# Kernel optimization log

Hardware: AMD Instinct MI355X
Metric: run time of the kernel (lower is better)

Reference implementation:

```python
import jax, jax.numpy as jnp
import numpy as np

B, Q, K, H = 8, 2048, 2048, 512


def setup_inputs() -> dict:
    key = jax.random.key(0)
    ks = jax.random.split(key, 12)
    s = 1.0 / np.sqrt(H)
    return {
        "query": jax.random.normal(ks[0], (B, Q, H), jnp.float32),
        "key_": jax.random.normal(ks[1], (B, K, H), jnp.float32),
        "value": jax.random.normal(ks[2], (B, K, H), jnp.float32),
        "mask": jax.random.randint(ks[3], (B, K), 0, 2).astype(bool),
        "Wq": jax.random.normal(ks[4], (H, H), jnp.float32) * s,
        "bq": jnp.zeros((H,), jnp.float32),
        "Wk": jax.random.normal(ks[5], (H, H), jnp.float32) * s,
        "bk": jnp.zeros((H,), jnp.float32),
        "Wv": jax.random.normal(ks[6], (H, H), jnp.float32) * s,
        "bv": jnp.zeros((H,), jnp.float32),
        "Wo": jax.random.normal(ks[7], (H, H), jnp.float32) * s,
        "bo": jnp.zeros((H,), jnp.float32),
    }


def reference(query, key_, value, mask, Wq, bq, Wk, bk, Wv, bv, Wo, bo):
    scale = jnp.sqrt(jnp.float32(H))
    Qp = query @ Wq + bq          # (B,Q,H)
    Kp = key_ @ Wk + bk           # (B,K,H)
    Vp = value @ Wv + bv          # (B,K,H)
    energy = jnp.einsum("bqh,bkh->bqk", Qp, Kp) / scale
    # mask is (B, key_len); torch code broadcasts it over all query rows
    energy = jnp.where(mask[:, None, :], -jnp.inf, energy)
    idx = jnp.argmax(energy, axis=-1)                 # (B,Q)
    score = jax.nn.one_hot(idx, K, dtype=energy.dtype)  # hardmax one-hot (B,Q,K)
    # score @ V is exactly a per-row gather of the argmax-selected V row
    res = jnp.take_along_axis(Vp, idx[:, :, None], axis=1)  # (B,Q,H)
    res = res @ Wo + bo
    return (res, score)
```

## Files before the change

kernel.cpp:

```cpp
#include <hip/hip_runtime.h>

typedef _Float16 f16;
typedef f16 f16x8 __attribute__((ext_vector_type(8)));
typedef f16 f16x4 __attribute__((ext_vector_type(4)));
typedef short s16x8 __attribute__((ext_vector_type(8)));
typedef short s16x4 __attribute__((ext_vector_type(4)));
typedef float f32x4 __attribute__((ext_vector_type(4)));

#define MFMA16(a,b,c)  __builtin_amdgcn_mfma_f32_16x16x32_f16(a,b,c,0,0,0)
#define MFMAB16(a,b,c) __builtin_amdgcn_mfma_f32_16x16x32_bf16(a,b,c,0,0,0)

static constexpr int Bn = 8, Qn = 2048, Kn = 2048, Hn = 512;
static constexpr int Mn = Bn * Qn;

typedef __attribute__((address_space(1))) const unsigned int as1_uint;
typedef __attribute__((address_space(3))) unsigned int as3_uint;

__device__ __forceinline__ void gl_lds16(const void* g, void* l) {
    __builtin_amdgcn_global_load_lds((as1_uint*)g, (as3_uint*)l, 16, 0, 0);
}

__device__ __forceinline__ short bf16r(float x) {
    unsigned u = __builtin_bit_cast(unsigned, x);
    u += 0x7fffu + ((u >> 16) & 1u);
    return (short)(u >> 16);
}

__device__ __forceinline__ int swz(int row) { return (row >> 1) & 3; }

__global__ __launch_bounds__(256) void compact_mask(
    const int* __restrict__ mask, int* __restrict__ cidx, int* __restrict__ cnt)
{
    __shared__ int sums[256];
    int b = blockIdx.x, t = threadIdx.x;
    int base = b * Kn + t * 8;
    int mv[8]; int s = 0;
    #pragma unroll
    for (int i = 0; i < 8; ++i) { mv[i] = (mask[base + i] == 0); s += mv[i]; }
    sums[t] = s;
    __syncthreads();
    for (int off = 1; off < 256; off <<= 1) {
        int v = (t >= off) ? sums[t - off] : 0;
        __syncthreads();
        sums[t] += v;
        __syncthreads();
    }
    int pos = (t > 0 ? sums[t - 1] : 0);
    #pragma unroll
    for (int i = 0; i < 8; ++i)
        if (mv[i]) cidx[b * Kn + pos++] = t * 8 + i;
    if (t == 255) {
        int total = sums[255];
        if (total == 0) { cidx[b * Kn] = 0; total = 1; }
        cnt[b] = total;
    }
}

__global__ __launch_bounds__(256) void prep_split(
    const float* __restrict__ Wk, const float* __restrict__ Wo,
    f16* __restrict__ Wk_h, f16* __restrict__ Wk_l, short* __restrict__ Wot)
{
    int e = blockIdx.x * 256 + threadIdx.x;
    float v = Wk[e] * 512.0f;
    f16 h = (f16)v;
    Wk_h[e] = h; Wk_l[e] = (f16)((v - (float)h) * 2048.0f);
    int r = e >> 9, c = e & 511;
    Wot[c * 512 + r] = bf16r(Wo[e]);
}

__global__ __launch_bounds__(512) void prep_vec(
    const float* __restrict__ Wk, const float* __restrict__ Wo,
    const float* __restrict__ bq, const float* __restrict__ bv,
    const float* __restrict__ bo,
    float* __restrict__ wvec, float* __restrict__ cvec)
{
    int t = threadIdx.x;
    float s = 0.f;
    for (int n = 0; n < 512; n += 4) {
        f32x4 a = *(const f32x4*)(Wk + (size_t)t * 512 + n);
        f32x4 q = *(const f32x4*)(bq + n);
        s += a[0]*q[0] + a[1]*q[1] + a[2]*q[2] + a[3]*q[3];
    }
    wvec[t] = s * (1.0f / 512.0f);
    float s2 = 0.f;
    for (int h = 0; h < 512; ++h) s2 += bv[h] * Wo[h * 512 + t];
    cvec[t] = s2 + bo[t];
}

template<int PREP>
__global__ __launch_bounds__(256) void gemm_split(
    const float* __restrict__ Af,
    const f16* __restrict__ Bh_g, const f16* __restrict__ Bl_g,
    f16* __restrict__ Oh, f16* __restrict__ Ol)
{
    __shared__ __align__(16) f16 Ah[2][2048], Al[2][2048], Bh[2][4096], Bl[2][4096];
    const int tid = threadIdx.x, lane = tid & 63, wid = tid >> 6;
    const int l15 = lane & 15, lg = lane >> 4;
    const int m0 = blockIdx.x * 64, n0 = blockIdx.y * 128;
    const int srow = lane >> 2, sg = lane & 3;
    const int ar0 = tid >> 3, ac0 = (tid & 7) * 4;

    auto stageB = [&](int buf, int ks) {
        const int k0 = ks << 5;
        #pragma unroll
        for (int h = 0; h < 2; ++h) {
            int s = wid + h * 4;
            int row = s * 16 + srow;
            int goff = k0 + ((sg ^ swz(row)) << 3);
            gl_lds16(Bh_g + (size_t)(n0 + row) * Hn + goff, &Bh[buf][s * 512]);
            gl_lds16(Bl_g + (size_t)(n0 + row) * Hn + goff, &Bl[buf][s * 512]);
        }
    };
    auto writeA = [&](int buf, const f32x4* av) {
        #pragma unroll
        for (int rr = 0; rr < 2; ++rr) {
            int row = ar0 + rr * 32;
            f16x4 oh, ol;
            #pragma unroll
            for (int j = 0; j < 4; ++j) {
                f16 hh = (f16)av[rr][j];
                oh[j] = hh;
                ol[j] = (f16)((av[rr][j] - (float)hh) * 2048.0f);
            }
            int off = row * 32 + (((ac0 >> 3) ^ swz(row)) << 3) + (ac0 & 7);
            *(f16x4*)&Ah[buf][off] = oh;
            *(f16x4*)&Al[buf][off] = ol;
        }
    };

    const float* aSrc[2];
    #pragma unroll
    for (int rr = 0; rr < 2; ++rr)
        aSrc[rr] = Af + (size_t)(m0 + ar0 + rr * 32) * Hn;

    f32x4 a0[4][2] = {}, a1[4][2] = {};
    {
        f32x4 av[2];
        #pragma unroll
        for (int rr = 0; rr < 2; ++rr) av[rr] = *(const f32x4*)(aSrc[rr] + ac0);
        stageB(0, 0);
        writeA(0, av);
    }
    __syncthreads();
    #pragma unroll 1
    for (int ks = 0; ks < 16; ++ks) {
        const int cur = ks & 1, nxt = cur ^ 1;
        f32x4 av[2];
        if (ks < 15) {
            const int k1 = (ks + 1) << 5;
            #pragma unroll
            for (int rr = 0; rr < 2; ++rr) av[rr] = *(const f32x4*)(aSrc[rr] + k1 + ac0);
            stageB(nxt, ks + 1);
        }
        f16x8 fbh[2], fbl[2];
        #pragma unroll
        for (int fj = 0; fj < 2; ++fj) {
            int row = wid * 32 + fj * 16 + l15;
            int off = row * 32 + ((lg ^ swz(row)) << 3);
            fbh[fj] = *(f16x8*)&Bh[cur][off];
            fbl[fj] = *(f16x8*)&Bl[cur][off];
        }
        #pragma unroll
        for (int fi = 0; fi < 4; ++fi) {
            int row = fi * 16 + l15;
            int off = row * 32 + ((lg ^ swz(row)) << 3);
            f16x8 fah = *(f16x8*)&Ah[cur][off];
            f16x8 fal = *(f16x8*)&Al[cur][off];
            #pragma unroll
            for (int fj = 0; fj < 2; ++fj) {
                a0[fi][fj] = MFMA16(fah, fbh[fj], a0[fi][fj]);
                a1[fi][fj] = MFMA16(fah, fbl[fj], a1[fi][fj]);
                a1[fi][fj] = MFMA16(fal, fbh[fj], a1[fi][fj]);
            }
        }
        if (ks < 15) writeA(nxt, av);
        __syncthreads();
    }
    #pragma unroll
    for (int fi = 0; fi < 4; ++fi)
    #pragma unroll
    for (int fj = 0; fj < 2; ++fj)
    #pragma unroll
    for (int j = 0; j < 4; ++j) {
        int m = m0 + fi * 16 + lg * 4 + j;
        int n = n0 + wid * 32 + fj * 16 + l15;
        float v = a0[fi][fj][j] + a1[fi][fj][j] * (1.0f / 2048.0f);
        if (PREP == 0) v *= (1.0f / 512.0f);
        f16 h = (f16)v;
        f16 lo = (f16)((v - (float)h) * 2048.0f);
        size_t o = PREP ? ((size_t)n * Hn + m) : ((size_t)m * Hn + n);
        Oh[o] = h; Ol[o] = lo;
    }
}

template<int MODE>
__global__ __launch_bounds__(256) void gemm_bfk(
    const float* __restrict__ Af, const short* __restrict__ Bt,
    const float* __restrict__ cvec, const int* __restrict__ idxArr,
    void* __restrict__ Out)
{
    __shared__ __align__(16) short As[2][2048], Bs[2][4096];
    const int tid = threadIdx.x, lane = tid & 63, wid = tid >> 6;
    const int l15 = lane & 15, lg = lane >> 4;
    const int m0 = blockIdx.x * 64, n0 = blockIdx.y * 128;
    const int srow = lane >> 2, sg = lane & 3;
    const int ar0 = tid >> 3, ac0 = (tid & 7) * 4;

    const float* aSrc[2];
    #pragma unroll
    for (int rr = 0; rr < 2; ++rr) {
        int row = ar0 + rr * 32;
        size_t grow;
        if (MODE == 1) {
            int b = m0 >> 11;
            grow = (size_t)(b * Kn + idxArr[m0 + row]);
        } else {
            grow = (size_t)(m0 + row);
        }
        aSrc[rr] = Af + grow * Hn;
    }

    auto stageB = [&](int buf, int ks) {
        const int k0 = ks << 5;
        #pragma unroll
        for (int h = 0; h < 2; ++h) {
            int s = wid + h * 4;
            int row = s * 16 + srow;
            int goff = k0 + ((sg ^ swz(row)) << 3);
            gl_lds16(Bt + (size_t)(n0 + row) * Hn + goff, &Bs[buf][s * 512]);
        }
    };
    auto writeA = [&](int buf, const f32x4* av) {
        #pragma unroll
        for (int rr = 0; rr < 2; ++rr) {
            int row = ar0 + rr * 32;
            s16x4 o;
            #pragma unroll
            for (int j = 0; j < 4; ++j) o[j] = bf16r(av[rr][j]);
            int off = row * 32 + (((ac0 >> 3) ^ swz(row)) << 3) + (ac0 & 7);
            *(s16x4*)&As[buf][off] = o;
        }
    };

    f32x4 acc[4][2] = {};
    {
        f32x4 av[2];
        #pragma unroll
        for (int rr = 0; rr < 2; ++rr) av[rr] = *(const f32x4*)(aSrc[rr] + ac0);
        stageB(0, 0);
        writeA(0, av);
    }
    __syncthreads();
    #pragma unroll 1
    for (int ks = 0; ks < 16; ++ks) {
        const int cur = ks & 1, nxt = cur ^ 1;
        f32x4 av[2];
        if (ks < 15) {
            const int k1 = (ks + 1) << 5;
            #pragma unroll
            for (int rr = 0; rr < 2; ++rr) av[rr] = *(const f32x4*)(aSrc[rr] + k1 + ac0);
            stageB(nxt, ks + 1);
        }
        s16x8 fb[2];
        #pragma unroll
        for (int fj = 0; fj < 2; ++fj) {
            int row = wid * 32 + fj * 16 + l15;
            fb[fj] = *(s16x8*)&Bs[cur][row * 32 + ((lg ^ swz(row)) << 3)];
        }
        #pragma unroll
        for (int fi = 0; fi < 4; ++fi) {
            int row = fi * 16 + l15;
            s16x8 fa = *(s16x8*)&As[cur][row * 32 + ((lg ^ swz(row)) << 3)];
            #pragma unroll
            for (int fj = 0; fj < 2; ++fj)
                acc[fi][fj] = MFMAB16(fa, fb[fj], acc[fi][fj]);
        }
        if (ks < 15) writeA(nxt, av);
        __syncthreads();
    }
    #pragma unroll
    for (int fi = 0; fi < 4; ++fi)
    #pragma unroll
    for (int fj = 0; fj < 2; ++fj)
    #pragma unroll
    for (int j = 0; j < 4; ++j) {
        int m = m0 + fi * 16 + lg * 4 + j;
        int n = n0 + wid * 32 + fj * 16 + l15;
        if (MODE == 0) {
            ((short*)Out)[(size_t)n * Hn + m] = bf16r(acc[fi][fj][j]);
        } else {
            ((float*)Out)[(size_t)m * Hn + n] = acc[fi][fj][j] + cvec[n];
        }
    }
}

__global__ __launch_bounds__(256) void kconv(
    const float* __restrict__ key_, const int* __restrict__ cidx,
    const int* __restrict__ cnt, const float* __restrict__ wvec,
    f16* __restrict__ Kc_h, float* __restrict__ beta)
{
    int wid = threadIdx.x >> 6, lane = threadIdx.x & 63;
    int b = blockIdx.y, j = blockIdx.x * 4 + wid;
    int cn = cnt[b];
    if (j >= cn) return;
    const float* src = key_ + (size_t)(b * Kn + cidx[b * Kn + j]) * Hn;
    size_t dst = (size_t)(b * Kn + j) * Hn;
    float s = 0.f;
    #pragma unroll
    for (int i = 0; i < 2; ++i) {
        int c0 = lane * 8 + i * 4;
        f32x4 v = *(const f32x4*)(src + c0);
        f32x4 w = *(const f32x4*)(wvec + c0);
        f16x4 oh;
        #pragma unroll
        for (int e = 0; e < 4; ++e) {
            oh[e] = (f16)v[e];
            s += v[e] * w[e];
        }
        *(f16x4*)(Kc_h + dst + c0) = oh;
    }
    #pragma unroll
    for (int sm = 1; sm < 64; sm <<= 1) s += __shfl_xor(s, sm, 64);
    if (lane == 0) beta[b * Kn + j] = s;
}

__global__ __launch_bounds__(256) void energy_approx(
    const f16* __restrict__ Qh, const f16* __restrict__ Kh,
    const float* __restrict__ beta, const int* __restrict__ cnt,
    f16* __restrict__ approxE)
{
    __shared__ __align__(16) f16 Ah[2][4096], Bh[2][4096];
    const int tid = threadIdx.x, lane = tid & 63, wid = tid >> 6;
    const int wr = wid >> 1, wc = wid & 1, l15 = lane & 15, lg = lane >> 4;
    const int qt = blockIdx.x, kc = blockIdx.y, b = blockIdx.z;
    const int cn = cnt[b];
    const int kbase = kc << 7;
    if (kbase >= cn) return;
    const int m0 = b * Qn + qt * 128;
    const int kr0 = b * Kn + kbase;
    const int srow = lane >> 2, sg = lane & 3;

    auto stage = [&](int buf, int ks) {
        const int k0 = ks << 5;
        #pragma unroll
        for (int h = 0; h < 2; ++h) {
            int s = wid + h * 4;
            int row = s * 16 + srow;
            int goff = k0 + ((sg ^ swz(row)) << 3);
            gl_lds16(Qh + (size_t)(m0 + row) * Hn + goff, &Ah[buf][s * 512]);
            gl_lds16(Kh + (size_t)(kr0 + row) * Hn + goff, &Bh[buf][s * 512]);
        }
    };

    f32x4 acc[4][4] = {};
    stage(0, 0);
    __syncthreads();
    #pragma unroll 1
    for (int ks = 0; ks < 16; ++ks) {
        const int cur = ks & 1;
        if (ks < 15) stage(cur ^ 1, ks + 1);
        f16x8 fb[4];
        #pragma unroll
        for (int fj = 0; fj < 4; ++fj) {
            int row = wc * 64 + fj * 16 + l15;
            fb[fj] = *(f16x8*)&Bh[cur][row * 32 + ((lg ^ swz(row)) << 3)];
        }
        #pragma unroll
        for (int fi = 0; fi < 4; ++fi) {
            int row = wr * 64 + fi * 16 + l15;
            f16x8 fa = *(f16x8*)&Ah[cur][row * 32 + ((lg ^ swz(row)) << 3)];
            #pragma unroll
            for (int fj = 0; fj < 4; ++fj)
                acc[fi][fj] = MFMA16(fa, fb[fj], acc[fi][fj]);
        }
        __syncthreads();
    }
    const f16 NEGI = (f16)(-__builtin_inff());
    float bet[4]; int valid[4];
    #pragma unroll
    for (int fj = 0; fj < 4; ++fj) {
        int lc = wc * 64 + fj * 16 + l15;
        valid[fj] = (kbase + lc < cn);
        bet[fj] = valid[fj] ? beta[b * Kn + kbase + lc] : 0.0f;
    }
    #pragma unroll
    for (int fi = 0; fi < 4; ++fi)
    #pragma unroll
    for (int fj = 0; fj < 4; ++fj)
    #pragma unroll
    for (int j = 0; j < 4; ++j) {
        int row = wr * 64 + fi * 16 + lg * 4 + j;
        int col = wc * 64 + fj * 16 + l15;
        f16 out = valid[fj] ? (f16)(acc[fi][fj][j] + bet[fj]) : NEGI;
        approxE[(size_t)(m0 + row) * Kn + kbase + col] = out;
    }
}

__global__ __launch_bounds__(256) void refine(
    const f16* __restrict__ approxE,
    const f16* __restrict__ qMh, const f16* __restrict__ qMl,
    const float* __restrict__ key_, const float* __restrict__ beta,
    const int* __restrict__ cidx, const int* __restrict__ cnt,
    int* __restrict__ idxArr)
{
    const int wid = threadIdx.x >> 6, lane = threadIdx.x & 63;
    const int m = blockIdx.x * 4 + wid;
    const int b = m >> 11;
    const int cn = cnt[b];
    const int nc128 = ((cn + 127) >> 7) << 7;
    const float NEGINF = -__builtin_inff();
    const f16* row = approxE + (size_t)m * Kn;

    f16x8 c[4];
    float fmaxv = NEGINF;
    #pragma unroll
    for (int g = 0; g < 4; ++g) {
        int cb = g * 512 + lane * 8;
        if (cb < nc128) {
            c[g] = *(const f16x8*)(row + cb);
            #pragma unroll
            for (int p = 0; p < 8; ++p) fmaxv = fmaxf(fmaxv, (float)c[g][p]);
        } else {
            #pragma unroll
            for (int p = 0; p < 8; ++p) c[g][p] = (f16)NEGINF;
        }
    }
    #pragma unroll
    for (int sm = 1; sm < 64; sm <<= 1) fmaxv = fmaxf(fmaxv, __shfl_xor(fmaxv, sm, 64));
    const float thr = fmaxv - 1.0f;

    float q8[8];
    int haveQ = 0;
    float bestV = NEGINF; int bestOrig = 0x7fffffff;
    int ncand = 0, firstJ = -1;

    #pragma unroll
    for (int g = 0; g < 4; ++g) {
        #pragma unroll
        for (int p = 0; p < 8; ++p) {
            unsigned long long mb = __ballot((float)c[g][p] >= thr);
            while (mb) {
                int L = __builtin_ctzll(mb);
                mb &= mb - 1;
                int j = g * 512 + L * 8 + p;
                ++ncand;
                if (ncand == 1) { firstJ = j; continue; }
                if (!haveQ) {
                    haveQ = 1;
                    int h0 = lane * 8;
                    f16x8 qh = *(const f16x8*)(qMh + (size_t)m * Hn + h0);
                    f16x8 ql = *(const f16x8*)(qMl + (size_t)m * Hn + h0);
                    #pragma unroll
                    for (int e = 0; e < 8; ++e)
                        q8[e] = (float)qh[e] + (float)ql[e] * (1.0f / 2048.0f);
                    int o1 = cidx[b * Kn + firstJ];
                    const float* kr = key_ + ((size_t)(b * Kn + o1)) * Hn + lane * 8;
                    float d = 0.f;
                    #pragma unroll
                    for (int e = 0; e < 8; ++e) d += q8[e] * kr[e];
                    #pragma unroll
                    for (int sm = 1; sm < 64; sm <<= 1) d += __shfl_xor(d, sm, 64);
                    d += beta[b * Kn + firstJ];
                    bestV = d; bestOrig = o1;
                }
                int orig = cidx[b * Kn + j];
                const float* kr = key_ + ((size_t)(b * Kn + orig)) * Hn + lane * 8;
                float d = 0.f;
                #pragma unroll
                for (int e = 0; e < 8; ++e) d += q8[e] * kr[e];
                #pragma unroll
                for (int sm = 1; sm < 64; sm <<= 1) d += __shfl_xor(d, sm, 64);
                d += beta[b * Kn + j];
                if (d > bestV || (d == bestV && orig < bestOrig)) { bestV = d; bestOrig = orig; }
            }
        }
    }
    if (ncand == 1) bestOrig = cidx[b * Kn + firstJ];
    if (lane == 0) idxArr[m] = bestOrig;
}

__global__ __launch_bounds__(256) void score_fill(
    const int* __restrict__ idxArr, float* __restrict__ score)
{
    int m = blockIdx.x;
    int c = idxArr[m];
    float* row = score + (size_t)m * Kn;
    int t = threadIdx.x;
    #pragma unroll
    for (int i = 0; i < 2; ++i) {
        int v = t + i * 256;
        f32x4 val = {0.f, 0.f, 0.f, 0.f};
        if ((c >> 2) == v) val[c & 3] = 1.0f;
        *(f32x4*)(row + v * 4) = val;
    }
}

extern "C" void kernel_launch(void* const* d_in, const int* in_sizes, int n_in,
                              void* d_out, int out_size, void* d_ws, size_t ws_size,
                              hipStream_t stream)
{
    const float* query = (const float*)d_in[0];
    const float* key_  = (const float*)d_in[1];
    const float* value = (const float*)d_in[2];
    const int*   mask  = (const int*)d_in[3];
    const float* Wq = (const float*)d_in[4];
    const float* bq = (const float*)d_in[5];
    const float* Wk = (const float*)d_in[6];
    const float* bv = (const float*)d_in[9];
    const float* Wv = (const float*)d_in[8];
    const float* Wo = (const float*)d_in[10];
    const float* bo = (const float*)d_in[11];

    float* res = (float*)d_out;
    float* scoreBase = res + (size_t)Mn * Hn;
    char* sc = (char*)scoreBase;
    constexpr size_t MB = 1u << 20;
    f16*   qM_h = (f16*)(sc + 0 * MB);
    f16*   qM_l = (f16*)(sc + 16 * MB);
    f16*   Kc_h = (f16*)(sc + 32 * MB);
    f16*   apxE = (f16*)(sc + 48 * MB);
    char*  wb   = sc + 112 * MB;
    f16*   Mt_h = (f16*)(wb);
    f16*   Mt_l = (f16*)(wb + 524288);
    f16*   Wk_h = (f16*)(wb + 2 * 524288);
    f16*   Wk_l = (f16*)(wb + 3 * 524288);
    short* Wot  = (short*)(wb + 4 * 524288);
    short* NtB  = (short*)(wb + 5 * 524288);
    float* wvec = (float*)(wb + 6 * 524288);
    float* cvec = (float*)(wb + 6 * 524288 + 4096);
    float* beta = (float*)(wb + 6 * 524288 + 8192);
    int*   cidx = (int*)(wb + 6 * 524288 + 8192 + 65536);

    int*   idxArr = (int*)d_ws;
    int*   cnt    = (int*)d_ws + Mn;

    compact_mask<<<Bn, 256, 0, stream>>>(mask, cidx, cnt);
    prep_split<<<1024, 256, 0, stream>>>(Wk, Wo, Wk_h, Wk_l, Wot);
    prep_vec<<<1, 512, 0, stream>>>(Wk, Wo, bq, bv, bo, wvec, cvec);

    gemm_split<1><<<dim3(8, 4), 256, 0, stream>>>(Wq, Wk_h, Wk_l, Mt_h, Mt_l);
    gemm_bfk<0><<<dim3(8, 4), 256, 0, stream>>>(Wv, Wot, nullptr, nullptr, NtB);
    gemm_split<0><<<dim3(Mn / 64, 4), 256, 0, stream>>>(query, Mt_h, Mt_l, qM_h, qM_l);
    kconv<<<dim3(512, Bn), 256, 0, stream>>>(key_, cidx, cnt, wvec, Kc_h, beta);

    energy_approx<<<dim3(Qn / 128, 16, Bn), 256, 0, stream>>>(
        qM_h, Kc_h, beta, cnt, apxE);

    refine<<<Mn / 4, 256, 0, stream>>>(
        apxE, qM_h, qM_l, key_, beta, cidx, cnt, idxArr);

    gemm_bfk<1><<<dim3(Mn / 64, 4), 256, 0, stream>>>(value, NtB, cvec, idxArr, res);

    score_fill<<<Mn, 256, 0, stream>>>(idxArr, scoreBase);
}
```

Baseline: 243.4 us.

## Fuse prep and tail kernels, add per-chunk argmax partials to energy pass

Merges the three prep kernels into one launch, fuses the query projection GEMM with the key conversion, and fuses the output GEMM with the one-hot score fill. The energy_approx kernel now also emits a per-128-column max and index for each row, so refine reads a few partials instead of scanning the full approximate-energy row. Refine only rereads the chunks that reach the threshold, and skips the exact dot products when there is a single candidate. This cuts launch count and the memory traffic in refine, at the cost of more complex kernels and a workspace layout that moves cvec and NtB into d_ws.

After: 246.3 us. About the same (+1.2%).

```diff
diff --git a/kernel.cpp b/kernel.cpp
--- a/kernel.cpp
+++ b/kernel.cpp
@@ -28,63 +28,62 @@
 
 __device__ __forceinline__ int swz(int row) { return (row >> 1) & 3; }
 
-__global__ __launch_bounds__(256) void compact_mask(
-    const int* __restrict__ mask, int* __restrict__ cidx, int* __restrict__ cnt)
-{
-    __shared__ int sums[256];
-    int b = blockIdx.x, t = threadIdx.x;
-    int base = b * Kn + t * 8;
-    int mv[8]; int s = 0;
-    #pragma unroll
-    for (int i = 0; i < 8; ++i) { mv[i] = (mask[base + i] == 0); s += mv[i]; }
-    sums[t] = s;
-    __syncthreads();
-    for (int off = 1; off < 256; off <<= 1) {
-        int v = (t >= off) ? sums[t - off] : 0;
-        __syncthreads();
-        sums[t] += v;
-        __syncthreads();
-    }
-    int pos = (t > 0 ? sums[t - 1] : 0);
-    #pragma unroll
-    for (int i = 0; i < 8; ++i)
-        if (mv[i]) cidx[b * Kn + pos++] = t * 8 + i;
-    if (t == 255) {
-        int total = sums[255];
-        if (total == 0) { cidx[b * Kn] = 0; total = 1; }
-        cnt[b] = total;
-    }
-}
-
-__global__ __launch_bounds__(256) void prep_split(
-    const float* __restrict__ Wk, const float* __restrict__ Wo,
-    f16* __restrict__ Wk_h, f16* __restrict__ Wk_l, short* __restrict__ Wot)
-{
-    int e = blockIdx.x * 256 + threadIdx.x;
-    float v = Wk[e] * 512.0f;
-    f16 h = (f16)v;
-    Wk_h[e] = h; Wk_l[e] = (f16)((v - (float)h) * 2048.0f);
-    int r = e >> 9, c = e & 511;
-    Wot[c * 512 + r] = bf16r(Wo[e]);
-}
-
-__global__ __launch_bounds__(512) void prep_vec(
-    const float* __restrict__ Wk, const float* __restrict__ Wo,
-    const float* __restrict__ bq, const float* __restrict__ bv,
-    const float* __restrict__ bo,
+__global__ __launch_bounds__(256) void prep_all(
+    const int* __restrict__ mask, const float* __restrict__ Wk,
+    const float* __restrict__ Wo, const float* __restrict__ bq,
+    const float* __restrict__ bv, const float* __restrict__ bo,
+    int* __restrict__ cidx, int* __restrict__ cnt,
+    f16* __restrict__ Wk_h, f16* __restrict__ Wk_l, short* __restrict__ Wot,
     float* __restrict__ wvec, float* __restrict__ cvec)
 {
-    int t = threadIdx.x;
-    float s = 0.f;
-    for (int n = 0; n < 512; n += 4) {
-        f32x4 a = *(const f32x4*)(Wk + (size_t)t * 512 + n);
-        f32x4 q = *(const f32x4*)(bq + n);
-        s += a[0]*q[0] + a[1]*q[1] + a[2]*q[2] + a[3]*q[3];
-    }
-    wvec[t] = s * (1.0f / 512.0f);
-    float s2 = 0.f;
-    for (int h = 0; h < 512; ++h) s2 += bv[h] * Wo[h * 512 + t];
-    cvec[t] = s2 + bo[t];
+    const int bid = blockIdx.x, t = threadIdx.x;
+    if (bid < 8) {
+        __shared__ int sums[256];
+        int b = bid;
+        int base = b * Kn + t * 8;
+        int mv[8]; int s = 0;
+        #pragma unroll
+        for (int i = 0; i < 8; ++i) { mv[i] = (mask[base + i] == 0); s += mv[i]; }
+        sums[t] = s;
+        __syncthreads();
+        for (int off = 1; off < 256; off <<= 1) {
+            int v = (t >= off) ? sums[t - off] : 0;
+            __syncthreads();
+            sums[t] += v;
+            __syncthreads();
+        }
+        int pos = (t > 0 ? sums[t - 1] : 0);
+        #pragma unroll
+        for (int i = 0; i < 8; ++i)
+            if (mv[i]) cidx[b * Kn + pos++] = t * 8 + i;
+        if (t == 255) {
+            int total = sums[255];
+            if (total == 0) { cidx[b * Kn] = 0; total = 1; }
+            cnt[b] = total;
+        }
+    } else if (bid < 1032) {
+        int e = (bid - 8) * 256 + t;
+        float v = Wk[e] * 512.0f;
+        f16 h = (f16)v;
+        Wk_h[e] = h; Wk_l[e] = (f16)((v - (float)h) * 2048.0f);
+        int r = e >> 9, c = e & 511;
+        Wot[c * 512 + r] = bf16r(Wo[e]);
+    } else {
+        #pragma unroll
+        for (int i = 0; i < 2; ++i) {
+            int tt = t + i * 256;
+            float s = 0.f;
+            for (int n = 0; n < 512; n += 4) {
+                f32x4 a = *(const f32x4*)(Wk + (size_t)tt * 512 + n);
+                f32x4 q = *(const f32x4*)(bq + n);
+                s += a[0]*q[0] + a[1]*q[1] + a[2]*q[2] + a[3]*q[3];
+            }
+            wvec[tt] = s * (1.0f / 512.0f);
+            float s2 = 0.f;
+            for (int h = 0; h < 512; ++h) s2 += bv[h] * Wo[h * 512 + tt];
+            cvec[tt] = s2 + bo[tt];
+        }
+    }
 }
 
 template<int PREP>
@@ -193,11 +192,9 @@
     }
 }
 
-template<int MODE>
-__global__ __launch_bounds__(256) void gemm_bfk(
+__global__ __launch_bounds__(256) void gemm_bfk0(
     const float* __restrict__ Af, const short* __restrict__ Bt,
-    const float* __restrict__ cvec, const int* __restrict__ idxArr,
-    void* __restrict__ Out)
+    short* __restrict__ Out)
 {
     __shared__ __align__(16) short As[2][2048], Bs[2][4096];
     const int tid = threadIdx.x, lane = tid & 63, wid = tid >> 6;
@@ -208,17 +205,8 @@
 
     const float* aSrc[2];
     #pragma unroll
-    for (int rr = 0; rr < 2; ++rr) {
-        int row = ar0 + rr * 32;
-        size_t grow;
-        if (MODE == 1) {
-            int b = m0 >> 11;
-            grow = (size_t)(b * Kn + idxArr[m0 + row]);
-        } else {
-            grow = (size_t)(m0 + row);
-        }
-        aSrc[rr] = Af + grow * Hn;
-    }
+    for (int rr = 0; rr < 2; ++rr)
+        aSrc[rr] = Af + (size_t)(m0 + ar0 + rr * 32) * Hn;
 
     auto stageB = [&](int buf, int ks) {
         const int k0 = ks << 5;
@@ -286,48 +274,157 @@
     for (int j = 0; j < 4; ++j) {
         int m = m0 + fi * 16 + lg * 4 + j;
         int n = n0 + wid * 32 + fj * 16 + l15;
-        if (MODE == 0) {
-            ((short*)Out)[(size_t)n * Hn + m] = bf16r(acc[fi][fj][j]);
-        } else {
-            ((float*)Out)[(size_t)m * Hn + n] = acc[fi][fj][j] + cvec[n];
-        }
-    }
-}
-
-__global__ __launch_bounds__(256) void kconv(
+        Out[(size_t)n * Hn + m] = bf16r(acc[fi][fj][j]);
+    }
+}
+
+__global__ __launch_bounds__(256) void qm_kconv(
+    const float* __restrict__ query,
+    const f16* __restrict__ Mt_h, const f16* __restrict__ Mt_l,
+    f16* __restrict__ qM_h, f16* __restrict__ qM_l,
     const float* __restrict__ key_, const int* __restrict__ cidx,
     const int* __restrict__ cnt, const float* __restrict__ wvec,
     f16* __restrict__ Kc_h, float* __restrict__ beta)
 {
-    int wid = threadIdx.x >> 6, lane = threadIdx.x & 63;
-    int b = blockIdx.y, j = blockIdx.x * 4 + wid;
-    int cn = cnt[b];
-    if (j >= cn) return;
-    const float* src = key_ + (size_t)(b * Kn + cidx[b * Kn + j]) * Hn;
-    size_t dst = (size_t)(b * Kn + j) * Hn;
-    float s = 0.f;
-    #pragma unroll
-    for (int i = 0; i < 2; ++i) {
-        int c0 = lane * 8 + i * 4;
-        f32x4 v = *(const f32x4*)(src + c0);
-        f32x4 w = *(const f32x4*)(wvec + c0);
-        f16x4 oh;
-        #pragma unroll
-        for (int e = 0; e < 4; ++e) {
-            oh[e] = (f16)v[e];
-            s += v[e] * w[e];
-        }
-        *(f16x4*)(Kc_h + dst + c0) = oh;
-    }
-    #pragma unroll
-    for (int sm = 1; sm < 64; sm <<= 1) s += __shfl_xor(s, sm, 64);
-    if (lane == 0) beta[b * Kn + j] = s;
+    __shared__ __align__(16) f16 smem[2][2048 + 2048 + 4096 + 4096];
+    const int bid = blockIdx.x;
+    const int tid = threadIdx.x, lane = tid & 63, wid = tid >> 6;
+    if (bid < 1024) {
+        f16 (*Ah)[2048+2048+4096+4096] = smem;
+        #define AH(b,i) Ah[b][i]
+        #define AL(b,i) Ah[b][2048 + (i)]
+        #define BH(b,i) Ah[b][4096 + (i)]
+        #define BL(b,i) Ah[b][8192 + (i)]
+        const int l15 = lane & 15, lg = lane >> 4;
+        const int m0 = (bid & 255) * 64, n0 = (bid >> 8) * 128;
+        const int srow = lane >> 2, sg = lane & 3;
+        const int ar0 = tid >> 3, ac0 = (tid & 7) * 4;
+
+        auto stageB = [&](int buf, int ks) {
+            const int k0 = ks << 5;
+            #pragma unroll
+            for (int h = 0; h < 2; ++h) {
+                int s = wid + h * 4;
+                int row = s * 16 + srow;
+                int goff = k0 + ((sg ^ swz(row)) << 3);
+                gl_lds16(Mt_h + (size_t)(n0 + row) * Hn + goff, &BH(buf, s * 512));
+                gl_lds16(Mt_l + (size_t)(n0 + row) * Hn + goff, &BL(buf, s * 512));
+            }
+        };
+        auto writeA = [&](int buf, const f32x4* av) {
+            #pragma unroll
+            for (int rr = 0; rr < 2; ++rr) {
+                int row = ar0 + rr * 32;
+                f16x4 oh, ol;
+                #pragma unroll
+                for (int j = 0; j < 4; ++j) {
+                    f16 hh = (f16)av[rr][j];
+                    oh[j] = hh;
+                    ol[j] = (f16)((av[rr][j] - (float)hh) * 2048.0f);
+                }
+                int off = row * 32 + (((ac0 >> 3) ^ swz(row)) << 3) + (ac0 & 7);
+                *(f16x4*)&AH(buf, off) = oh;
+                *(f16x4*)&AL(buf, off) = ol;
+            }
+        };
+
+        const float* aSrc[2];
+        #pragma unroll
+        for (int rr = 0; rr < 2; ++rr)
+            aSrc[rr] = query + (size_t)(m0 + ar0 + rr * 32) * Hn;
+
+        f32x4 a0[4][2] = {}, a1[4][2] = {};
+        {
+            f32x4 av[2];
+            #pragma unroll
+            for (int rr = 0; rr < 2; ++rr) av[rr] = *(const f32x4*)(aSrc[rr] + ac0);
+            stageB(0, 0);
+            writeA(0, av);
+        }
+        __syncthreads();
+        #pragma unroll 1
+        for (int ks = 0; ks < 16; ++ks) {
+            const int cur = ks & 1, nxt = cur ^ 1;
+            f32x4 av[2];
+            if (ks < 15) {
+                const int k1 = (ks + 1) << 5;
+                #pragma unroll
+                for (int rr = 0; rr < 2; ++rr) av[rr] = *(const f32x4*)(aSrc[rr] + k1 + ac0);
+                stageB(nxt, ks + 1);
+            }
+            f16x8 fbh[2], fbl[2];
+            #pragma unroll
+            for (int fj = 0; fj < 2; ++fj) {
+                int row = wid * 32 + fj * 16 + l15;
+                int off = row * 32 + ((lg ^ swz(row)) << 3);
+                fbh[fj] = *(f16x8*)&BH(cur, off);
+                fbl[fj] = *(f16x8*)&BL(cur, off);
+            }
+            #pragma unroll
+            for (int fi = 0; fi < 4; ++fi) {
+                int row = fi * 16 + l15;
+                int off = row * 32 + ((lg ^ swz(row)) << 3);
+                f16x8 fah = *(f16x8*)&AH(cur, off);
+                f16x8 fal = *(f16x8*)&AL(cur, off);
+                #pragma unroll
+                for (int fj = 0; fj < 2; ++fj) {
+                    a0[fi][fj] = MFMA16(fah, fbh[fj], a0[fi][fj]);
+                    a1[fi][fj] = MFMA16(fah, fbl[fj], a1[fi][fj]);
+                    a1[fi][fj] = MFMA16(fal, fbh[fj], a1[fi][fj]);
+                }
+            }
+            if (ks < 15) writeA(nxt, av);
+            __syncthreads();
+        }
+        #pragma unroll
+        for (int fi = 0; fi < 4; ++fi)
+        #pragma unroll
+        for (int fj = 0; fj < 2; ++fj)
+        #pragma unroll
+        for (int j = 0; j < 4; ++j) {
+            int m = m0 + fi * 16 + lg * 4 + j;
+            int n = n0 + wid * 32 + fj * 16 + l15;
+            float v = (a0[fi][fj][j] + a1[fi][fj][j] * (1.0f / 2048.0f)) * (1.0f / 512.0f);
+            f16 h = (f16)v;
+            qM_h[(size_t)m * Hn + n] = h;
+            qM_l[(size_t)m * Hn + n] = (f16)((v - (float)h) * 2048.0f);
+        }
+        #undef AH
+        #undef AL
+        #undef BH
+        #undef BL
+    } else {
+        int kb = bid - 1024;
+        int b = kb >> 9;
+        int j = (kb & 511) * 4 + wid;
+        int cn = cnt[b];
+        if (j >= cn) return;
+        const float* src = key_ + (size_t)(b * Kn + cidx[b * Kn + j]) * Hn;
+        size_t dst = (size_t)(b * Kn + j) * Hn;
+        float s = 0.f;
+        #pragma unroll
+        for (int i = 0; i < 2; ++i) {
+            int c0 = lane * 8 + i * 4;
+            f32x4 v = *(const f32x4*)(src + c0);
+            f32x4 w = *(const f32x4*)(wvec + c0);
+            f16x4 oh;
+            #pragma unroll
+            for (int e = 0; e < 4; ++e) {
+                oh[e] = (f16)v[e];
+                s += v[e] * w[e];
+            }
+            *(f16x4*)(Kc_h + dst + c0) = oh;
+        }
+        #pragma unroll
+        for (int sm = 1; sm < 64; sm <<= 1) s += __shfl_xor(s, sm, 64);
+        if (lane == 0) beta[b * Kn + j] = s;
+    }
 }
 
 __global__ __launch_bounds__(256) void energy_approx(
     const f16* __restrict__ Qh, const f16* __restrict__ Kh,
     const float* __restrict__ beta, const int* __restrict__ cnt,
-    f16* __restrict__ approxE)
+    f16* __restrict__ approxE, float* __restrict__ pval, int* __restrict__ pidx)
 {
     __shared__ __align__(16) f16 Ah[2][4096], Bh[2][4096];
     const int tid = threadIdx.x, lane = tid & 63, wid = tid >> 6;
@@ -339,6 +436,7 @@
     const int m0 = b * Qn + qt * 128;
     const int kr0 = b * Kn + kbase;
     const int srow = lane >> 2, sg = lane & 3;
+    const float NEGINF = -__builtin_inff();
 
     auto stage = [&](int buf, int ks) {
         const int k0 = ks << 5;
@@ -375,7 +473,7 @@
         }
         __syncthreads();
     }
-    const f16 NEGI = (f16)(-__builtin_inff());
+    const f16 NEGI = (f16)NEGINF;
     float bet[4]; int valid[4];
     #pragma unroll
     for (int fj = 0; fj < 4; ++fj) {
@@ -383,21 +481,47 @@
         valid[fj] = (kbase + lc < cn);
         bet[fj] = valid[fj] ? beta[b * Kn + kbase + lc] : 0.0f;
     }
+    float (*bwv)[128] = (float(*)[128])&Ah[0][0];
+    int   (*bwi)[128] = (int(*)[128])&Ah[1][0];
     #pragma unroll
     for (int fi = 0; fi < 4; ++fi)
     #pragma unroll
-    for (int fj = 0; fj < 4; ++fj)
-    #pragma unroll
     for (int j = 0; j < 4; ++j) {
-        int row = wr * 64 + fi * 16 + lg * 4 + j;
-        int col = wc * 64 + fj * 16 + l15;
-        f16 out = valid[fj] ? (f16)(acc[fi][fj][j] + bet[fj]) : NEGI;
-        approxE[(size_t)(m0 + row) * Kn + kbase + col] = out;
+        float bv = NEGINF; int bc = 0x7fffffff;
+        #pragma unroll
+        for (int fj = 0; fj < 4; ++fj) {
+            int lc = wc * 64 + fj * 16 + l15;
+            float v = valid[fj] ? (acc[fi][fj][j] + bet[fj]) : NEGINF;
+            int row = wr * 64 + fi * 16 + lg * 4 + j;
+            approxE[(size_t)(m0 + row) * Kn + kbase + lc] = valid[fj] ? (f16)v : NEGI;
+            if (v > bv || (v == bv && lc < bc)) { bv = v; bc = lc; }
+        }
+        #pragma unroll
+        for (int sm = 1; sm < 16; sm <<= 1) {
+            float ov = __shfl_xor(bv, sm, 64);
+            int   oc = __shfl_xor(bc, sm, 64);
+            if (ov > bv || (ov == bv && oc < bc)) { bv = ov; bc = oc; }
+        }
+        if (l15 == 0) {
+            int row = wr * 64 + fi * 16 + lg * 4 + j;
+            bwv[wc][row] = bv; bwi[wc][row] = bc;
+        }
+    }
+    __syncthreads();
+    if (tid < 128) {
+        float v0 = bwv[0][tid], v1 = bwv[1][tid];
+        int   i0 = bwi[0][tid], i1 = bwi[1][tid];
+        float v; int i;
+        if (v0 > v1 || (v0 == v1 && i0 < i1)) { v = v0; i = i0; } else { v = v1; i = i1; }
+        int m = m0 + tid;
+        pval[m * 16 + kc] = v;
+        pidx[m * 16 + kc] = kbase + i;
     }
 }
 
 __global__ __launch_bounds__(256) void refine(
-    const f16* __restrict__ approxE,
+    const f16* __restrict__ apxE, const float* __restrict__ pval,
+    const int* __restrict__ pidx,
     const f16* __restrict__ qMh, const f16* __restrict__ qMl,
     const float* __restrict__ key_, const float* __restrict__ beta,
     const int* __restrict__ cidx, const int* __restrict__ cnt,
@@ -407,62 +531,55 @@
     const int m = blockIdx.x * 4 + wid;
     const int b = m >> 11;
     const int cn = cnt[b];
-    const int nc128 = ((cn + 127) >> 7) << 7;
+    const int nch = (cn + 127) >> 7;
     const float NEGINF = -__builtin_inff();
-    const f16* row = approxE + (size_t)m * Kn;
-
-    f16x8 c[4];
-    float fmaxv = NEGINF;
-    #pragma unroll
-    for (int g = 0; g < 4; ++g) {
-        int cb = g * 512 + lane * 8;
-        if (cb < nc128) {
-            c[g] = *(const f16x8*)(row + cb);
-            #pragma unroll
-            for (int p = 0; p < 8; ++p) fmaxv = fmaxf(fmaxv, (float)c[g][p]);
-        } else {
-            #pragma unroll
-            for (int p = 0; p < 8; ++p) c[g][p] = (f16)NEGINF;
-        }
-    }
-    #pragma unroll
-    for (int sm = 1; sm < 64; sm <<= 1) fmaxv = fmaxf(fmaxv, __shfl_xor(fmaxv, sm, 64));
-    const float thr = fmaxv - 1.0f;
-
+
+    float chv = (lane < nch) ? pval[m * 16 + lane] : NEGINF;
+    int   chi = (lane < nch) ? pidx[m * 16 + lane] : 0x7fffffff;
+    float gv = chv; int gi = chi;
+    #pragma unroll
+    for (int sm = 1; sm < 64; sm <<= 1) {
+        float ov = __shfl_xor(gv, sm, 64);
+        int   oc = __shfl_xor(gi, sm, 64);
+        if (ov > gv || (ov == gv && oc < gi)) { gv = ov; gi = oc; }
+    }
+    const float thr = gv - 1.0f;
+
+    int ncand = 0;
+    for (int c = 0; c < nch; ++c) {
+        float cmax = __shfl(chv, c, 64);
+        if (cmax < thr) continue;
+        const f16* ap = apxE + (size_t)m * Kn + c * 128 + lane * 2;
+        ncand += __popcll(__ballot((float)ap[0] >= thr));
+        ncand += __popcll(__ballot((float)ap[1] >= thr));
+    }
+    if (ncand == 1) {
+        if (lane == 0) idxArr[m] = cidx[b * Kn + gi];
+        return;
+    }
     float q8[8];
-    int haveQ = 0;
+    {
+        f16x8 qh = *(const f16x8*)(qMh + (size_t)m * Hn + lane * 8);
+        f16x8 ql = *(const f16x8*)(qMl + (size_t)m * Hn + lane * 8);
+        #pragma unroll
+        for (int e = 0; e < 8; ++e)
+            q8[e] = (float)qh[e] + (float)ql[e] * (1.0f / 2048.0f);
+    }
     float bestV = NEGINF; int bestOrig = 0x7fffffff;
-    int ncand = 0, firstJ = -1;
-
-    #pragma unroll
-    for (int g = 0; g < 4; ++g) {
-        #pragma unroll
-        for (int p = 0; p < 8; ++p) {
-            unsigned long long mb = __ballot((float)c[g][p] >= thr);
+    for (int c = 0; c < nch; ++c) {
+        float cmax = __shfl(chv, c, 64);
+        if (cmax < thr) continue;
+        const f16* ap = apxE + (size_t)m * Kn + c * 128 + lane * 2;
+        unsigned long long bb[2];
+        bb[0] = __ballot((float)ap[0] >= thr);
+        bb[1] = __ballot((float)ap[1] >= thr);
+        #pragma unroll
+        for (int p = 0; p < 2; ++p) {
+            unsigned long long mb = bb[p];
             while (mb) {
                 int L = __builtin_ctzll(mb);
                 mb &= mb - 1;
-                int j = g * 512 + L * 8 + p;
-                ++ncand;
-                if (ncand == 1) { firstJ = j; continue; }
-                if (!haveQ) {
-                    haveQ = 1;
-                    int h0 = lane * 8;
-                    f16x8 qh = *(const f16x8*)(qMh + (size_t)m * Hn + h0);
-                    f16x8 ql = *(const f16x8*)(qMl + (size_t)m * Hn + h0);
-                    #pragma unroll
-                    for (int e = 0; e < 8; ++e)
-                        q8[e] = (float)qh[e] + (float)ql[e] * (1.0f / 2048.0f);
-                    int o1 = cidx[b * Kn + firstJ];
-                    const float* kr = key_ + ((size_t)(b * Kn + o1)) * Hn + lane * 8;
-                    float d = 0.f;
-                    #pragma unroll
-                    for (int e = 0; e < 8; ++e) d += q8[e] * kr[e];
-                    #pragma unroll
-                    for (int sm = 1; sm < 64; sm <<= 1) d += __shfl_xor(d, sm, 64);
-                    d += beta[b * Kn + firstJ];
-                    bestV = d; bestOrig = o1;
-                }
+                int j = c * 128 + L * 2 + p;
                 int orig = cidx[b * Kn + j];
                 const float* kr = key_ + ((size_t)(b * Kn + orig)) * Hn + lane * 8;
                 float d = 0.f;
@@ -475,23 +592,110 @@
             }
         }
     }
-    if (ncand == 1) bestOrig = cidx[b * Kn + firstJ];
     if (lane == 0) idxArr[m] = bestOrig;
 }
 
-__global__ __launch_bounds__(256) void score_fill(
-    const int* __restrict__ idxArr, float* __restrict__ score)
+__global__ __launch_bounds__(256) void tail_fused(
+    const float* __restrict__ value, const short* __restrict__ NtB,
+    const float* __restrict__ cvec, const int* __restrict__ idxArr,
+    float* __restrict__ res, float* __restrict__ score)
 {
-    int m = blockIdx.x;
-    int c = idxArr[m];
-    float* row = score + (size_t)m * Kn;
-    int t = threadIdx.x;
-    #pragma unroll
-    for (int i = 0; i < 2; ++i) {
-        int v = t + i * 256;
-        f32x4 val = {0.f, 0.f, 0.f, 0.f};
-        if ((c >> 2) == v) val[c & 3] = 1.0f;
-        *(f32x4*)(row + v * 4) = val;
+    __shared__ __align__(16) short As[2][2048], Bs[2][4096];
+    const int bid = blockIdx.x;
+    const int tid = threadIdx.x, lane = tid & 63, wid = tid >> 6;
+    if (bid >= 1024) {
+        int m = bid - 1024;
+        int c = idxArr[m];
+        float* row = score + (size_t)m * Kn;
+        #pragma unroll
+        for (int i = 0; i < 2; ++i) {
+            int v = tid + i * 256;
+            f32x4 val = {0.f, 0.f, 0.f, 0.f};
+            if ((c >> 2) == v) val[c & 3] = 1.0f;
+            *(f32x4*)(row + v * 4) = val;
+        }
+        return;
+    }
+    const int l15 = lane & 15, lg = lane >> 4;
+    const int m0 = (bid & 255) * 64, n0 = (bid >> 8) * 128;
+    const int srow = lane >> 2, sg = lane & 3;
+    const int ar0 = tid >> 3, ac0 = (tid & 7) * 4;
+
+    const float* aSrc[2];
+    #pragma unroll
+    for (int rr = 0; rr < 2; ++rr) {
+        int row = ar0 + rr * 32;
+        int bb = m0 >> 11;
+        aSrc[rr] = value + (size_t)(bb * Kn + idxArr[m0 + row]) * Hn;
+    }
+
+    auto stageB = [&](int buf, int ks) {
+        const int k0 = ks << 5;
+        #pragma unroll
+        for (int h = 0; h < 2; ++h) {
+            int s = wid + h * 4;
+            int row = s * 16 + srow;
+            int goff = k0 + ((sg ^ swz(row)) << 3);
+            gl_lds16(NtB + (size_t)(n0 + row) * Hn + goff, &Bs[buf][s * 512]);
+        }
+    };
+    auto writeA = [&](int buf, const f32x4* av) {
+        #pragma unroll
+        for (int rr = 0; rr < 2; ++rr) {
+            int row = ar0 + rr * 32;
+            s16x4 o;
+            #pragma unroll
+            for (int j = 0; j < 4; ++j) o[j] = bf16r(av[rr][j]);
+            int off = row * 32 + (((ac0 >> 3) ^ swz(row)) << 3) + (ac0 & 7);
+            *(s16x4*)&As[buf][off] = o;
+        }
+    };
+
+    f32x4 acc[4][2] = {};
+    {
+        f32x4 av[2];
+        #pragma unroll
+        for (int rr = 0; rr < 2; ++rr) av[rr] = *(const f32x4*)(aSrc[rr] + ac0);
+        stageB(0, 0);
+        writeA(0, av);
+    }
+    __syncthreads();
+    #pragma unroll 1
+    for (int ks = 0; ks < 16; ++ks) {
+        const int cur = ks & 1, nxt = cur ^ 1;
+        f32x4 av[2];
+        if (ks < 15) {
+            const int k1 = (ks + 1) << 5;
+            #pragma unroll
+            for (int rr = 0; rr < 2; ++rr) av[rr] = *(const f32x4*)(aSrc[rr] + k1 + ac0);
+            stageB(nxt, ks + 1);
+        }
+        s16x8 fb[2];
+        #pragma unroll
+        for (int fj = 0; fj < 2; ++fj) {
+            int row = wid * 32 + fj * 16 + l15;
+            fb[fj] = *(s16x8*)&Bs[cur][row * 32 + ((lg ^ swz(row)) << 3)];
+        }
+        #pragma unroll
+        for (int fi = 0; fi < 4; ++fi) {
+            int row = fi * 16 + l15;
+            s16x8 fa = *(s16x8*)&As[cur][row * 32 + ((lg ^ swz(row)) << 3)];
+            #pragma unroll
+            for (int fj = 0; fj < 2; ++fj)
+                acc[fi][fj] = MFMAB16(fa, fb[fj], acc[fi][fj]);
+        }
+        if (ks < 15) writeA(nxt, av);
+        __syncthreads();
+    }
+    #pragma unroll
+    for (int fi = 0; fi < 4; ++fi)
+    #pragma unroll
+    for (int fj = 0; fj < 2; ++fj)
+    #pragma unroll
+    for (int j = 0; j < 4; ++j) {
+        int m = m0 + fi * 16 + lg * 4 + j;
+        int n = n0 + wid * 32 + fj * 16 + l15;
+        res[(size_t)m * Hn + n] = acc[fi][fj][j] + cvec[n];
     }
 }
 
@@ -525,31 +729,32 @@
     f16*   Wk_h = (f16*)(wb + 2 * 524288);
     f16*   Wk_l = (f16*)(wb + 3 * 524288);
     short* Wot  = (short*)(wb + 4 * 524288);
-    short* NtB  = (short*)(wb + 5 * 524288);
-    float* wvec = (float*)(wb + 6 * 524288);
-    float* cvec = (float*)(wb + 6 * 524288 + 4096);
-    float* beta = (float*)(wb + 6 * 524288 + 8192);
-    int*   cidx = (int*)(wb + 6 * 524288 + 8192 + 65536);
+    float* wvec = (float*)(wb + 5 * 524288);
+    float* beta = (float*)(wb + 5 * 524288 + 8192);
+    int*   cidx = (int*)(wb + 5 * 524288 + 8192 + 65536);
+    float* pval = (float*)(wb + 6 * 524288);
+    int*   pidx = (int*)(wb + 8 * 524288);
 
     int*   idxArr = (int*)d_ws;
-    int*   cnt    = (int*)d_ws + Mn;
-
-    compact_mask<<<Bn, 256, 0, stream>>>(mask, cidx, cnt);
-    prep_split<<<1024, 256, 0, stream>>>(Wk, Wo, Wk_h, Wk_l, Wot);
-    prep_vec<<<1, 512, 0, stream>>>(Wk, Wo, bq, bv, bo, wvec, cvec);
+    int*   cnt    = (int*)d_ws + 16384;
+    float* cvec   = (float*)((char*)d_ws + 65600);
+    short* NtB    = (short*)((char*)d_ws + 67648);
+
+    prep_all<<<1033, 256, 0, stream>>>(mask, Wk, Wo, bq, bv, bo,
+                                       cidx, cnt, Wk_h, Wk_l, Wot, wvec, cvec);
 
     gemm_split<1><<<dim3(8, 4), 256, 0, stream>>>(Wq, Wk_h, Wk_l, Mt_h, Mt_l);
-    gemm_bfk<0><<<dim3(8, 4), 256, 0, stream>>>(Wv, Wot, nullptr, nullptr, NtB);
-    gemm_split<0><<<dim3(Mn / 64, 4), 256, 0, stream>>>(query, Mt_h, Mt_l, qM_h, qM_l);
-    kconv<<<dim3(512, Bn), 256, 0, stream>>>(key_, cidx, cnt, wvec, Kc_h, beta);
+    gemm_bfk0<<<dim3(8, 4), 256, 0, stream>>>(Wv, Wot, NtB);
+
+    qm_kconv<<<5120, 256, 0, stream>>>(query, Mt_h, Mt_l, qM_h, qM_l,
+                                       key_, cidx, cnt, wvec, Kc_h, beta);
 
     energy_approx<<<dim3(Qn / 128, 16, Bn), 256, 0, stream>>>(
-        qM_h, Kc_h, beta, cnt, apxE);
+        qM_h, Kc_h, beta, cnt, apxE, pval, pidx);
 
     refine<<<Mn / 4, 256, 0, stream>>>(
-        apxE, qM_h, qM_l, key_, beta, cidx, cnt, idxArr);
-
-    gemm_bfk<1><<<dim3(Mn / 64, 4), 256, 0, stream>>>(value, NtB, cvec, idxArr, res);
-
-    score_fill<<<Mn, 256, 0, stream>>>(idxArr, scoreBase);
-}
+        apxE, pval, pidx, qM_h, qM_l, key_, beta, cidx, cnt, idxArr);
+
+    tail_fused<<<1024 + Mn, 256, 0, stream>>>(value, NtB, cvec, idxArr,
+                                              res, scoreBase);
+}
```
